# Performance work log

Hardware: AMD Instinct MI355X
Metric: run time of the kernel (lower is better)

The kernel has to match this reference:

```python
import jax, jax.numpy as jnp
import numpy as np

BLOCK_SIZE = 1024
DILATIONS = (1, 2, 4, 8)


def setup_inputs() -> dict:
    key = jax.random.key(0)
    kq, kk, kv, kw, kb = jax.random.split(key, 5)
    b, h, L, hd = 4, 8, 4096, 64
    hidden = h * hd
    return {
        "query_states": jax.random.normal(kq, (b, h, L, hd), jnp.float32),
        "key_states": jax.random.normal(kk, (b, h, L, hd), jnp.float32),
        "value_states": jax.random.normal(kv, (b, h, L, hd), jnp.float32),
        "Wo": jax.random.normal(kw, (hidden, hidden), jnp.float32),
        "bo": jax.random.normal(kb, (hidden,), jnp.float32),
    }


def _dilated_branch(q, k, v, d):
    """One dilation pass: strided gather -> block attention.
    Returns de (bsz, nh, Ld, 1) detached exp-row-sums and a (bsz, nh, Ld, hd)."""
    b, h, L, hd = q.shape
    qs, ks, vs = q[:, :, ::d], k[:, :, ::d], v[:, :, ::d]
    Ld = qs.shape[2]
    bs = min(BLOCK_SIZE, Ld)          # torch.split: one short block if Ld < block_size
    nb = Ld // bs                      # even split for chosen q_len
    blk = lambda x: x.reshape(b, h, nb, bs, hd)
    qb, kb, vb = blk(qs), blk(ks), blk(vs)
    scores = jnp.einsum('bhnqd,bhnkd->bhnqk', qb, kb) / jnp.sqrt(jnp.float32(hd))
    # detached, unstabilized exp-sum (matches attn_weights.detach().exp().sum(-1))
    de = jax.lax.stop_gradient(jnp.exp(scores).sum(-1, keepdims=True)).reshape(b, h, Ld, 1)
    probs = jax.nn.softmax(scores.astype(jnp.float32), axis=-1).astype(q.dtype)
    a = jnp.einsum('bhnqk,bhnkd->bhnqd', probs, vb).reshape(b, h, Ld, hd)
    return de, a


def reference(query_states, key_states, value_states, Wo, bo):
    b, h, L, hd = query_states.shape
    w = jnp.zeros((b, h, L, 1), jnp.float32)
    des, rs = [], []
    for d in DILATIONS:
        de, a = _dilated_branch(query_states, key_states, value_states, d)
        des.append(de)
        rs.append(a)
        w = w.at[:, :, ::d].add(de)
    out = jnp.zeros_like(query_states)
    for d, de, a in zip(DILATIONS, des, rs):
        aw = de / w[:, :, ::d]                     # (b, h, Ld, 1) relative weight
        out = out.at[:, :, ::d].add((aw * a).astype(query_states.dtype))
    out = out.transpose(0, 2, 1, 3).reshape(b, L, h * hd)
    return out @ Wo.T + bo
```

## Files before the change

kernel.cpp:

```cpp
#include <hip/hip_runtime.h>
#include <hip/hip_bf16.h>

typedef __attribute__((ext_vector_type(8))) short bf16x8;
typedef __attribute__((ext_vector_type(4))) float f32x4;
typedef unsigned short u16;

union F8 { bf16x8 v; unsigned u[4]; u16 s[8]; uint4 q; };

__device__ __forceinline__ unsigned pk2(float a, float b) {
    __hip_bfloat162 t = __float22bfloat162_rn(make_float2(a, b));
    unsigned r; __builtin_memcpy(&r, &t, 4); return r;
}
__device__ __forceinline__ u16 f2bf(float a) {
    __hip_bfloat16 t = __float2bfloat16(a);
    u16 r; __builtin_memcpy(&r, &t, 2); return r;
}
__device__ __forceinline__ float bf2f(u16 s) {
    unsigned u = ((unsigned)s) << 16; float f; __builtin_memcpy(&f, &u, 4); return f;
}
#define SWZ(byteoff, row) ((byteoff) ^ (((row) & 7) << 4))
#define MFMA(a, b, c) __builtin_amdgcn_mfma_f32_16x16x32_bf16((a), (b), (c), 0, 0, 0)

__global__ __launch_bounds__(256)
void prep_kernel(const float* __restrict__ K, const float* __restrict__ V,
                 u16* __restrict__ Kb, u16* __restrict__ Vt)
{
    __shared__ __align__(16) char tl[64 * 128];
    int blk = blockIdx.x;
    const int t = threadIdx.x;

    if (blk < 2048) {
        const int bh = blk >> 6, qt = blk & 63;
        const int q = qt * 64 + (t >> 2), dd0 = (t & 3) * 16;
        const float* kp = K + ((size_t)bh * 4096 + q) * 64 + dd0;
        float4 x0 = ((const float4*)kp)[0], x1 = ((const float4*)kp)[1];
        float4 x2 = ((const float4*)kp)[2], x3 = ((const float4*)kp)[3];
        F8 f0, f1;
        f0.u[0] = pk2(x0.x, x0.y); f0.u[1] = pk2(x0.z, x0.w);
        f0.u[2] = pk2(x1.x, x1.y); f0.u[3] = pk2(x1.z, x1.w);
        f1.u[0] = pk2(x2.x, x2.y); f1.u[1] = pk2(x2.z, x2.w);
        f1.u[2] = pk2(x3.x, x3.y); f1.u[3] = pk2(x3.z, x3.w);
        u16* op = Kb + ((size_t)bh * 4096 + q) * 64 + dd0;
        ((uint4*)op)[0] = f0.q; ((uint4*)op)[1] = f1.q;
        return;
    }
    blk -= 2048;
    int d, Ld; size_t vtoff;
    if (blk < 2048)      { d = 1; Ld = 4096; vtoff = 0; }
    else if (blk < 3072) { blk -= 2048; d = 2; Ld = 2048; vtoff = 8388608; }
    else if (blk < 3584) { blk -= 3072; d = 4; Ld = 1024; vtoff = 12582912; }
    else                 { blk -= 3584; d = 8; Ld = 512;  vtoff = 14680064; }
    const int tpb = Ld >> 6;
    const int bh = blk / tpb, jt = blk % tpb;
    {
        const int j = t >> 2, dd0 = (t & 3) * 16;
        const int q = (jt * 64 + j) * d;
        const float* vp = V + ((size_t)bh * 4096 + q) * 64 + dd0;
        float4 x0 = ((const float4*)vp)[0], x1 = ((const float4*)vp)[1];
        float4 x2 = ((const float4*)vp)[2], x3 = ((const float4*)vp)[3];
        F8 f0, f1;
        f0.u[0] = pk2(x0.x, x0.y); f0.u[1] = pk2(x0.z, x0.w);
        f0.u[2] = pk2(x1.x, x1.y); f0.u[3] = pk2(x1.z, x1.w);
        f1.u[0] = pk2(x2.x, x2.y); f1.u[1] = pk2(x2.z, x2.w);
        f1.u[2] = pk2(x3.x, x3.y); f1.u[3] = pk2(x3.z, x3.w);
        *(uint4*)(tl + SWZ(j * 128 + dd0 * 2, j)) = f0.q;
        *(uint4*)(tl + SWZ(j * 128 + dd0 * 2 + 16, j)) = f1.q;
    }
    __syncthreads();
    {
        const int dd = t >> 2, jb = (t & 3) * 16;
        F8 f0, f1;
#pragma unroll
        for (int i = 0; i < 8; ++i) {
            f0.s[i] = *(const u16*)(tl + SWZ((jb + i) * 128 + dd * 2, jb + i));
            f1.s[i] = *(const u16*)(tl + SWZ((jb + 8 + i) * 128 + dd * 2, jb + 8 + i));
        }
        u16* op = Vt + vtoff + ((size_t)bh * 64 + dd) * Ld + jt * 64 + jb;
        ((uint4*)op)[0] = f0.q; ((uint4*)op)[1] = f1.q;
    }
}

__global__ __launch_bounds__(256)
void attn_fused(const float* __restrict__ Q, const u16* __restrict__ Kb,
                const u16* __restrict__ Vt, float* __restrict__ num,
                float* __restrict__ wsum)
{
    const int L = 4096;
    const int per = gridDim.x >> 3;
    const int wg0 = blockIdx.x;
    const int wg = (wg0 & 7) * per + (wg0 >> 3);

    int d, npb, bs, rel; size_t vtoff;
    if (wg < 1024)      { d = 1; npb = 32; bs = 1024; rel = wg;        vtoff = 0; }
    else if (wg < 1536) { d = 2; npb = 16; bs = 1024; rel = wg - 1024; vtoff = 8388608; }
    else if (wg < 1792) { d = 4; npb = 8;  bs = 1024; rel = wg - 1536; vtoff = 12582912; }
    else                { d = 8; npb = 4;  bs = 512;  rel = wg - 1792; vtoff = 14680064; }

    const int bh = rel / npb;
    const int qt = rel % npb;
    const int b = bh >> 3, h = bh & 7;
    const int tid = threadIdx.x;
    const int w = tid >> 6, lane = tid & 63;
    const int g = lane >> 4, c = lane & 15;
    const int bstart = ((qt * 128) / bs) * bs;
    const int qrow0 = qt * 128 + w * 32;
    const int Ld = npb * 128;

    __shared__ __align__(16) char smem[32 * 1024];
    char* const Kls = smem;
    char* const Vls = smem + 8192;
    char* const Pls = smem + 16384 + w * 4096;

    const size_t base = (size_t)bh * L * 64;
    const size_t vbase = vtoff + (size_t)bh * 64 * Ld;
    const float qs = 0.125f * 1.44269504088896341f;

    bf16x8 qf[2][2];
#pragma unroll
    for (int qi = 0; qi < 2; ++qi) {
        const float* qp = Q + base + (size_t)(qrow0 + qi * 16 + c) * d * 64 + g * 8;
#pragma unroll
        for (int s = 0; s < 2; ++s) {
            float4 x = ((const float4*)(qp + s * 32))[0];
            float4 y = ((const float4*)(qp + s * 32))[1];
            F8 f;
            f.u[0] = pk2(x.x * qs, x.y * qs);
            f.u[1] = pk2(x.z * qs, x.w * qs);
            f.u[2] = pk2(y.x * qs, y.y * qs);
            f.u[3] = pk2(y.z * qs, y.w * qs);
            qf[qi][s] = f.v;
        }
    }

    f32x4 o[2][4];
#pragma unroll
    for (int qi = 0; qi < 2; ++qi)
#pragma unroll
        for (int dj = 0; dj < 4; ++dj) o[qi][dj] = (f32x4){0.f, 0.f, 0.f, 0.f};
    float lrow[2] = {0.f, 0.f};

    const int krow = tid >> 2, kc = tid & 3;

    uint4 ka, kb2, va, vb;
    {
        const u16* kp = Kb + base + (size_t)(bstart + krow) * d * 64 + kc * 16;
        ka = ((const uint4*)kp)[0]; kb2 = ((const uint4*)kp)[1];
        const u16* vp = Vt + vbase + (size_t)lane * Ld + bstart + w * 16;
        va = ((const uint4*)vp)[0]; vb = ((const uint4*)vp)[1];
    }

    for (int kt = 0; kt < bs; kt += 64) {
        *(uint4*)(Kls + SWZ(krow * 128 + kc * 32, krow)) = ka;
        *(uint4*)(Kls + SWZ(krow * 128 + kc * 32 + 16, krow)) = kb2;
        *(uint4*)(Vls + SWZ(lane * 128 + w * 32, lane)) = va;
        *(uint4*)(Vls + SWZ(lane * 128 + w * 32 + 16, lane)) = vb;
        __syncthreads();

        if (kt + 64 < bs) {
            const u16* kp = Kb + base + (size_t)(bstart + kt + 64 + krow) * d * 64 + kc * 16;
            ka = ((const uint4*)kp)[0]; kb2 = ((const uint4*)kp)[1];
            const u16* vp = Vt + vbase + (size_t)lane * Ld + bstart + kt + 64 + w * 16;
            va = ((const uint4*)vp)[0]; vb = ((const uint4*)vp)[1];
        }

        f32x4 st[2][4];
#pragma unroll
        for (int kj = 0; kj < 4; ++kj) {
            const int row = 16 * kj + c;
            bf16x8 kf0 = *(const bf16x8*)(Kls + SWZ(row * 128 + g * 16, row));
            bf16x8 kf1 = *(const bf16x8*)(Kls + SWZ(row * 128 + 64 + g * 16, row));
            f32x4 z = (f32x4){0.f, 0.f, 0.f, 0.f};
            st[0][kj] = MFMA(kf1, qf[0][1], MFMA(kf0, qf[0][0], z));
            st[1][kj] = MFMA(kf1, qf[1][1], MFMA(kf0, qf[1][0], z));
        }

#pragma unroll
        for (int qi = 0; qi < 2; ++qi) {
            const int prow = 16 * qi + c;
            float rs = 0.f;
#pragma unroll
            for (int kj = 0; kj < 4; ++kj) {
                const float p0 = exp2f(st[qi][kj][0]);
                const float p1 = exp2f(st[qi][kj][1]);
                const float p2 = exp2f(st[qi][kj][2]);
                const float p3 = exp2f(st[qi][kj][3]);
                rs += (p0 + p1) + (p2 + p3);
                uint2 pv; pv.x = pk2(p0, p1); pv.y = pk2(p2, p3);
                *(uint2*)(Pls + SWZ(prow * 128 + kj * 32 + g * 8, prow)) = pv;
            }
            lrow[qi] += rs;
        }

#pragma unroll
        for (int s = 0; s < 2; ++s) {
            bf16x8 vf[4], pf[2];
#pragma unroll
            for (int dj = 0; dj < 4; ++dj) {
                const int row = 16 * dj + c;
                vf[dj] = *(const bf16x8*)(Vls + SWZ(row * 128 + s * 64 + g * 16, row));
            }
#pragma unroll
            for (int qi = 0; qi < 2; ++qi) {
                const int row = 16 * qi + c;
                pf[qi] = *(const bf16x8*)(Pls + SWZ(row * 128 + s * 64 + g * 16, row));
            }
#pragma unroll
            for (int qi = 0; qi < 2; ++qi)
#pragma unroll
                for (int dj = 0; dj < 4; ++dj)
                    o[qi][dj] = MFMA(pf[qi], vf[dj], o[qi][dj]);
        }
        __syncthreads();
    }

#pragma unroll
    for (int qi = 0; qi < 2; ++qi) {
        float lq = lrow[qi];
        lq += __shfl_xor(lq, 16);
        lq += __shfl_xor(lq, 32);
#pragma unroll
        for (int r = 0; r < 4; ++r) {
            const int q = qrow0 + 16 * qi + 4 * g + r;
            float* np = num + ((size_t)b * L + (size_t)q * d) * 512 + h * 64 + c;
#pragma unroll
            for (int dj = 0; dj < 4; ++dj)
                atomicAdd(np + dj * 16, o[qi][dj][r]);
        }
        if (g == 0) {
            const int q2 = qrow0 + 16 * qi + c;
            atomicAdd(wsum + ((size_t)b * L + (size_t)q2 * d) * 8 + h, lq);
        }
    }
}

__global__ __launch_bounds__(256)
void proj_mfma(const float* __restrict__ num, const float* __restrict__ wsum,
               const float* __restrict__ Wo, const float* __restrict__ bo,
               float* __restrict__ out)
{
    __shared__ __align__(16) char smem[64 * 1024];
    char* const Ah = smem;
    char* const Al = smem + 16384;
    char* const Bh = smem + 32768;
    char* const Bl = smem + 49152;

    const int tid = threadIdx.x;
    const int w = tid >> 6, lane = tid & 63, g = lane >> 4, c = lane & 15;
    const int wm = (w >> 1) * 64, wn = (w & 1) * 64;
    const int per = gridDim.x >> 3;
    const int wg0 = blockIdx.x;
    const int wg = (wg0 & 7) * per + (wg0 >> 3);
    const int bm = (wg >> 2) * 128, bn = (wg & 3) * 128;
    const int srow = tid >> 1, koff = (tid & 1) * 32;

    f32x4 acc[4][4];
#pragma unroll
    for (int mi = 0; mi < 4; ++mi)
#pragma unroll
        for (int ni = 0; ni < 4; ++ni) acc[mi][ni] = (f32x4){0.f, 0.f, 0.f, 0.f};

    for (int bk = 0; bk < 512; bk += 64) {
        {
            const float* ap = num + (size_t)(bm + srow) * 512 + bk + koff;
            const float winv = 1.0f / wsum[(size_t)(bm + srow) * 8 + (bk >> 6)];
#pragma unroll
            for (int i = 0; i < 8; ++i) {
                float4 a4 = ((const float4*)ap)[i];
                float v0 = a4.x * winv, v1 = a4.y * winv, v2 = a4.z * winv, v3 = a4.w * winv;
                u16 h0 = f2bf(v0), h1 = f2bf(v1), h2 = f2bf(v2), h3 = f2bf(v3);
                uint2 hi; hi.x = h0 | ((unsigned)h1 << 16); hi.y = h2 | ((unsigned)h3 << 16);
                uint2 lo;
                lo.x = f2bf(v0 - bf2f(h0)) | ((unsigned)f2bf(v1 - bf2f(h1)) << 16);
                lo.y = f2bf(v2 - bf2f(h2)) | ((unsigned)f2bf(v3 - bf2f(h3)) << 16);
                const int off = SWZ(srow * 128 + koff * 2 + i * 8, srow);
                *(uint2*)(Ah + off) = hi;
                *(uint2*)(Al + off) = lo;
            }
            const float* bp = Wo + (size_t)(bn + srow) * 512 + bk + koff;
#pragma unroll
            for (int i = 0; i < 8; ++i) {
                float4 a4 = ((const float4*)bp)[i];
                u16 h0 = f2bf(a4.x), h1 = f2bf(a4.y), h2 = f2bf(a4.z), h3 = f2bf(a4.w);
                uint2 hi; hi.x = h0 | ((unsigned)h1 << 16); hi.y = h2 | ((unsigned)h3 << 16);
                uint2 lo;
                lo.x = f2bf(a4.x - bf2f(h0)) | ((unsigned)f2bf(a4.y - bf2f(h1)) << 16);
                lo.y = f2bf(a4.z - bf2f(h2)) | ((unsigned)f2bf(a4.w - bf2f(h3)) << 16);
                const int off = SWZ(srow * 128 + koff * 2 + i * 8, srow);
                *(uint2*)(Bh + off) = hi;
                *(uint2*)(Bl + off) = lo;
            }
        }
        __syncthreads();
#pragma unroll
        for (int s = 0; s < 2; ++s) {
            bf16x8 ah[4], al[4], bh[4], bl[4];
#pragma unroll
            for (int mi = 0; mi < 4; ++mi) {
                const int row = wm + 16 * mi + c;
                const int off = SWZ(row * 128 + s * 64 + g * 16, row);
                ah[mi] = *(const bf16x8*)(Ah + off);
                al[mi] = *(const bf16x8*)(Al + off);
            }
#pragma unroll
            for (int ni = 0; ni < 4; ++ni) {
                const int row = wn + 16 * ni + c;
                const int off = SWZ(row * 128 + s * 64 + g * 16, row);
                bh[ni] = *(const bf16x8*)(Bh + off);
                bl[ni] = *(const bf16x8*)(Bl + off);
            }
#pragma unroll
            for (int mi = 0; mi < 4; ++mi)
#pragma unroll
                for (int ni = 0; ni < 4; ++ni) {
                    acc[mi][ni] = MFMA(ah[mi], bh[ni], acc[mi][ni]);
                    acc[mi][ni] = MFMA(ah[mi], bl[ni], acc[mi][ni]);
                    acc[mi][ni] = MFMA(al[mi], bh[ni], acc[mi][ni]);
                }
        }
        __syncthreads();
    }

    float bias[4];
#pragma unroll
    for (int ni = 0; ni < 4; ++ni) bias[ni] = bo[bn + wn + 16 * ni + c];
#pragma unroll
    for (int mi = 0; mi < 4; ++mi)
#pragma unroll
        for (int r = 0; r < 4; ++r) {
            float* op = out + (size_t)(bm + wm + 16 * mi + 4 * g + r) * 512 + bn + wn + c;
#pragma unroll
            for (int ni = 0; ni < 4; ++ni)
                op[ni * 16] = acc[mi][ni][r] + bias[ni];
        }
}

extern "C" void kernel_launch(void* const* d_in, const int* in_sizes, int n_in,
                              void* d_out, int out_size, void* d_ws, size_t ws_size,
                              hipStream_t stream)
{
    const float* Q  = (const float*)d_in[0];
    const float* K  = (const float*)d_in[1];
    const float* V  = (const float*)d_in[2];
    const float* Wo = (const float*)d_in[3];
    const float* bo = (const float*)d_in[4];
    float* out = (float*)d_out;

    float* num  = (float*)d_ws;
    float* wsum = num + (size_t)8388608;
    u16*  Kb    = (u16*)((char*)d_ws + 34078720);
    u16*  Vt    = (u16*)((char*)d_ws + 50855936);

    hipMemsetAsync(d_ws, 0, 34078720, stream);

    hipLaunchKernelGGL(prep_kernel, dim3(5888), dim3(256), 0, stream, K, V, Kb, Vt);
    hipLaunchKernelGGL(attn_fused, dim3(1920), dim3(256), 0, stream,
                       Q, Kb, Vt, num, wsum);
    hipLaunchKernelGGL(proj_mfma, dim3(512), dim3(256), 0, stream,
                       num, wsum, Wo, bo, out);
}
```

Before: 217.5 us.

## Switch attention to 32x32x16 MFMA with register P shuffle and double-buffered LDS

Rewrites the attention inner loop to use 32x32x16 bf16 MFMA tiles. The probability tile is now passed from the QK^T result into the PV operand through lane shuffles instead of a round trip through LDS. K/V LDS tiles are double-buffered with prefetch two steps ahead, leaving a single barrier per iteration. The aim is fewer LDS writes and reads, fewer MFMA issues, and fewer barriers. The cost is larger accumulator register use, extra shuffle/select work, and a different atomic write-out pattern.

```diff
diff --git a/kernel.cpp b/kernel.cpp
--- a/kernel.cpp
+++ b/kernel.cpp
@@ -3,6 +3,7 @@
 
 typedef __attribute__((ext_vector_type(8))) short bf16x8;
 typedef __attribute__((ext_vector_type(4))) float f32x4;
+typedef __attribute__((ext_vector_type(16))) float f32x16;
 typedef unsigned short u16;
 
 union F8 { bf16x8 v; unsigned u[4]; u16 s[8]; uint4 q; };
@@ -20,6 +21,7 @@
 }
 #define SWZ(byteoff, row) ((byteoff) ^ (((row) & 7) << 4))
 #define MFMA(a, b, c) __builtin_amdgcn_mfma_f32_16x16x32_bf16((a), (b), (c), 0, 0, 0)
+#define MFMA32(a, b, c) __builtin_amdgcn_mfma_f32_32x32x16_bf16((a), (b), (c), 0, 0, 0)
 
 __global__ __launch_bounds__(256)
 void prep_kernel(const float* __restrict__ K, const float* __restrict__ V,
@@ -101,136 +103,152 @@
     const int b = bh >> 3, h = bh & 7;
     const int tid = threadIdx.x;
     const int w = tid >> 6, lane = tid & 63;
-    const int g = lane >> 4, c = lane & 15;
+    const int lq = lane & 31;
+    const int hi = lane >> 5;
     const int bstart = ((qt * 128) / bs) * bs;
     const int qrow0 = qt * 128 + w * 32;
     const int Ld = npb * 128;
+    const int nt = bs >> 6;
 
     __shared__ __align__(16) char smem[32 * 1024];
-    char* const Kls = smem;
-    char* const Vls = smem + 8192;
-    char* const Pls = smem + 16384 + w * 4096;
-
     const size_t base = (size_t)bh * L * 64;
     const size_t vbase = vtoff + (size_t)bh * 64 * Ld;
     const float qs = 0.125f * 1.44269504088896341f;
 
-    bf16x8 qf[2][2];
-#pragma unroll
-    for (int qi = 0; qi < 2; ++qi) {
-        const float* qp = Q + base + (size_t)(qrow0 + qi * 16 + c) * d * 64 + g * 8;
-#pragma unroll
-        for (int s = 0; s < 2; ++s) {
-            float4 x = ((const float4*)(qp + s * 32))[0];
-            float4 y = ((const float4*)(qp + s * 32))[1];
+    bf16x8 qb[4];
+    {
+        const float* qp = Q + base + (size_t)(qrow0 + lq) * d * 64 + hi * 8;
+#pragma unroll
+        for (int ks = 0; ks < 4; ++ks) {
+            float4 x = ((const float4*)(qp + ks * 16))[0];
+            float4 y = ((const float4*)(qp + ks * 16))[1];
             F8 f;
             f.u[0] = pk2(x.x * qs, x.y * qs);
             f.u[1] = pk2(x.z * qs, x.w * qs);
             f.u[2] = pk2(y.x * qs, y.y * qs);
             f.u[3] = pk2(y.z * qs, y.w * qs);
-            qf[qi][s] = f.v;
-        }
-    }
-
-    f32x4 o[2][4];
-#pragma unroll
-    for (int qi = 0; qi < 2; ++qi)
-#pragma unroll
-        for (int dj = 0; dj < 4; ++dj) o[qi][dj] = (f32x4){0.f, 0.f, 0.f, 0.f};
-    float lrow[2] = {0.f, 0.f};
+            qb[ks] = f.v;
+        }
+    }
+
+    f32x16 o0, o1;
+#pragma unroll
+    for (int i = 0; i < 16; ++i) { o0[i] = 0.f; o1[i] = 0.f; }
+    float lrow = 0.f;
 
     const int krow = tid >> 2, kc = tid & 3;
 
     uint4 ka, kb2, va, vb;
+    const u16* kp0 = Kb + base + (size_t)(bstart + krow) * d * 64 + kc * 16;
+    const u16* vp0 = Vt + vbase + (size_t)lane * Ld + bstart + w * 16;
+    const size_t kstep = (size_t)64 * d * 64;
+
+    ka = ((const uint4*)kp0)[0]; kb2 = ((const uint4*)kp0)[1];
+    va = ((const uint4*)vp0)[0]; vb = ((const uint4*)vp0)[1];
     {
-        const u16* kp = Kb + base + (size_t)(bstart + krow) * d * 64 + kc * 16;
-        ka = ((const uint4*)kp)[0]; kb2 = ((const uint4*)kp)[1];
-        const u16* vp = Vt + vbase + (size_t)lane * Ld + bstart + w * 16;
-        va = ((const uint4*)vp)[0]; vb = ((const uint4*)vp)[1];
-    }
-
-    for (int kt = 0; kt < bs; kt += 64) {
+        char* Kls = smem; char* Vls = smem + 8192;
         *(uint4*)(Kls + SWZ(krow * 128 + kc * 32, krow)) = ka;
         *(uint4*)(Kls + SWZ(krow * 128 + kc * 32 + 16, krow)) = kb2;
         *(uint4*)(Vls + SWZ(lane * 128 + w * 32, lane)) = va;
         *(uint4*)(Vls + SWZ(lane * 128 + w * 32 + 16, lane)) = vb;
+    }
+    if (nt > 1) {
+        ka = ((const uint4*)(kp0 + kstep))[0]; kb2 = ((const uint4*)(kp0 + kstep))[1];
+        va = ((const uint4*)(vp0 + 64))[0];    vb = ((const uint4*)(vp0 + 64))[1];
+    }
+    __syncthreads();
+
+    for (int t = 0; t < nt; ++t) {
+        char* const Kls = smem + (t & 1) * 16384;
+        char* const Vls = Kls + 8192;
+        if (t + 1 < nt) {
+            char* Klsn = smem + ((t + 1) & 1) * 16384;
+            char* Vlsn = Klsn + 8192;
+            *(uint4*)(Klsn + SWZ(krow * 128 + kc * 32, krow)) = ka;
+            *(uint4*)(Klsn + SWZ(krow * 128 + kc * 32 + 16, krow)) = kb2;
+            *(uint4*)(Vlsn + SWZ(lane * 128 + w * 32, lane)) = va;
+            *(uint4*)(Vlsn + SWZ(lane * 128 + w * 32 + 16, lane)) = vb;
+        }
+        if (t + 2 < nt) {
+            const u16* kp = kp0 + (size_t)(t + 2) * kstep;
+            const u16* vp = vp0 + (t + 2) * 64;
+            ka = ((const uint4*)kp)[0]; kb2 = ((const uint4*)kp)[1];
+            va = ((const uint4*)vp)[0]; vb = ((const uint4*)vp)[1];
+        }
+
+        f32x16 st0, st1;
+#pragma unroll
+        for (int i = 0; i < 16; ++i) { st0[i] = 0.f; st1[i] = 0.f; }
+#pragma unroll
+        for (int ks = 0; ks < 4; ++ks) {
+            bf16x8 kf0 = *(const bf16x8*)(Kls + SWZ(lq * 128 + ks * 32 + hi * 16, lq));
+            bf16x8 kf1 = *(const bf16x8*)(Kls + SWZ((32 + lq) * 128 + ks * 32 + hi * 16, 32 + lq));
+            st0 = MFMA32(kf0, qb[ks], st0);
+            st1 = MFMA32(kf1, qb[ks], st1);
+        }
+
+        f32x16 p0, p1;
+        float rs = 0.f;
+#pragma unroll
+        for (int r = 0; r < 16; ++r) {
+            p0[r] = exp2f(st0[r]); p1[r] = exp2f(st1[r]);
+            rs += p0[r] + p1[r];
+        }
+        lrow += rs;
+
+        bf16x8 pa[4];
+        {
+            unsigned u0 = pk2(p0[0], p0[1]),   u1 = pk2(p0[2], p0[3]);
+            unsigned u2 = pk2(p0[4], p0[5]),   u3 = pk2(p0[6], p0[7]);
+            unsigned u4 = pk2(p0[8], p0[9]),   u5 = pk2(p0[10], p0[11]);
+            unsigned u6 = pk2(p0[12], p0[13]), u7 = pk2(p0[14], p0[15]);
+            unsigned t0 = __shfl_xor(u0, 32), t1 = __shfl_xor(u1, 32);
+            unsigned t2 = __shfl_xor(u2, 32), t3 = __shfl_xor(u3, 32);
+            unsigned t4 = __shfl_xor(u4, 32), t5 = __shfl_xor(u5, 32);
+            unsigned t6 = __shfl_xor(u6, 32), t7 = __shfl_xor(u7, 32);
+            F8 f;
+            f.u[0] = hi ? t2 : u0; f.u[1] = hi ? t3 : u1;
+            f.u[2] = hi ? u2 : t0; f.u[3] = hi ? u3 : t1;
+            pa[0] = f.v;
+            f.u[0] = hi ? t6 : u4; f.u[1] = hi ? t7 : u5;
+            f.u[2] = hi ? u6 : t4; f.u[3] = hi ? u7 : t5;
+            pa[1] = f.v;
+            u0 = pk2(p1[0], p1[1]);   u1 = pk2(p1[2], p1[3]);
+            u2 = pk2(p1[4], p1[5]);   u3 = pk2(p1[6], p1[7]);
+            u4 = pk2(p1[8], p1[9]);   u5 = pk2(p1[10], p1[11]);
+            u6 = pk2(p1[12], p1[13]); u7 = pk2(p1[14], p1[15]);
+            t0 = __shfl_xor(u0, 32); t1 = __shfl_xor(u1, 32);
+            t2 = __shfl_xor(u2, 32); t3 = __shfl_xor(u3, 32);
+            t4 = __shfl_xor(u4, 32); t5 = __shfl_xor(u5, 32);
+            t6 = __shfl_xor(u6, 32); t7 = __shfl_xor(u7, 32);
+            f.u[0] = hi ? t2 : u0; f.u[1] = hi ? t3 : u1;
+            f.u[2] = hi ? u2 : t0; f.u[3] = hi ? u3 : t1;
+            pa[2] = f.v;
+            f.u[0] = hi ? t6 : u4; f.u[1] = hi ? t7 : u5;
+            f.u[2] = hi ? u6 : t4; f.u[3] = hi ? u7 : t5;
+            pa[3] = f.v;
+        }
+
+#pragma unroll
+        for (int ks = 0; ks < 4; ++ks) {
+            bf16x8 v0 = *(const bf16x8*)(Vls + SWZ(lq * 128 + ks * 32 + hi * 16, lq));
+            bf16x8 v1 = *(const bf16x8*)(Vls + SWZ((32 + lq) * 128 + ks * 32 + hi * 16, 32 + lq));
+            o0 = MFMA32(pa[ks], v0, o0);
+            o1 = MFMA32(pa[ks], v1, o1);
+        }
         __syncthreads();
-
-        if (kt + 64 < bs) {
-            const u16* kp = Kb + base + (size_t)(bstart + kt + 64 + krow) * d * 64 + kc * 16;
-            ka = ((const uint4*)kp)[0]; kb2 = ((const uint4*)kp)[1];
-            const u16* vp = Vt + vbase + (size_t)lane * Ld + bstart + kt + 64 + w * 16;
-            va = ((const uint4*)vp)[0]; vb = ((const uint4*)vp)[1];
-        }
-
-        f32x4 st[2][4];
-#pragma unroll
-        for (int kj = 0; kj < 4; ++kj) {
-            const int row = 16 * kj + c;
-            bf16x8 kf0 = *(const bf16x8*)(Kls + SWZ(row * 128 + g * 16, row));
-            bf16x8 kf1 = *(const bf16x8*)(Kls + SWZ(row * 128 + 64 + g * 16, row));
-            f32x4 z = (f32x4){0.f, 0.f, 0.f, 0.f};
-            st[0][kj] = MFMA(kf1, qf[0][1], MFMA(kf0, qf[0][0], z));
-            st[1][kj] = MFMA(kf1, qf[1][1], MFMA(kf0, qf[1][0], z));
-        }
-
-#pragma unroll
-        for (int qi = 0; qi < 2; ++qi) {
-            const int prow = 16 * qi + c;
-            float rs = 0.f;
-#pragma unroll
-            for (int kj = 0; kj < 4; ++kj) {
-                const float p0 = exp2f(st[qi][kj][0]);
-                const float p1 = exp2f(st[qi][kj][1]);
-                const float p2 = exp2f(st[qi][kj][2]);
-                const float p3 = exp2f(st[qi][kj][3]);
-                rs += (p0 + p1) + (p2 + p3);
-                uint2 pv; pv.x = pk2(p0, p1); pv.y = pk2(p2, p3);
-                *(uint2*)(Pls + SWZ(prow * 128 + kj * 32 + g * 8, prow)) = pv;
-            }
-            lrow[qi] += rs;
-        }
-
-#pragma unroll
-        for (int s = 0; s < 2; ++s) {
-            bf16x8 vf[4], pf[2];
-#pragma unroll
-            for (int dj = 0; dj < 4; ++dj) {
-                const int row = 16 * dj + c;
-                vf[dj] = *(const bf16x8*)(Vls + SWZ(row * 128 + s * 64 + g * 16, row));
-            }
-#pragma unroll
-            for (int qi = 0; qi < 2; ++qi) {
-                const int row = 16 * qi + c;
-                pf[qi] = *(const bf16x8*)(Pls + SWZ(row * 128 + s * 64 + g * 16, row));
-            }
-#pragma unroll
-            for (int qi = 0; qi < 2; ++qi)
-#pragma unroll
-                for (int dj = 0; dj < 4; ++dj)
-                    o[qi][dj] = MFMA(pf[qi], vf[dj], o[qi][dj]);
-        }
-        __syncthreads();
-    }
-
-#pragma unroll
-    for (int qi = 0; qi < 2; ++qi) {
-        float lq = lrow[qi];
-        lq += __shfl_xor(lq, 16);
-        lq += __shfl_xor(lq, 32);
-#pragma unroll
-        for (int r = 0; r < 4; ++r) {
-            const int q = qrow0 + 16 * qi + 4 * g + r;
-            float* np = num + ((size_t)b * L + (size_t)q * d) * 512 + h * 64 + c;
-#pragma unroll
-            for (int dj = 0; dj < 4; ++dj)
-                atomicAdd(np + dj * 16, o[qi][dj][r]);
-        }
-        if (g == 0) {
-            const int q2 = qrow0 + 16 * qi + c;
-            atomicAdd(wsum + ((size_t)b * L + (size_t)q2 * d) * 8 + h, lq);
-        }
-    }
+    }
+
+    float lsum = lrow + __shfl_xor(lrow, 32);
+#pragma unroll
+    for (int r = 0; r < 16; ++r) {
+        const int qr = (r & 3) + 8 * (r >> 2) + 4 * hi;
+        float* np = num + ((size_t)b * L + (size_t)(qrow0 + qr) * d) * 512 + h * 64 + lq;
+        atomicAdd(np, o0[r]);
+        atomicAdd(np + 32, o1[r]);
+    }
+    if (lane < 32)
+        atomicAdd(wsum + ((size_t)b * L + (size_t)(qrow0 + lq) * d) * 8 + h, lsum);
 }
 
 __global__ __launch_bounds__(256)
@@ -268,12 +286,12 @@
                 float4 a4 = ((const float4*)ap)[i];
                 float v0 = a4.x * winv, v1 = a4.y * winv, v2 = a4.z * winv, v3 = a4.w * winv;
                 u16 h0 = f2bf(v0), h1 = f2bf(v1), h2 = f2bf(v2), h3 = f2bf(v3);
-                uint2 hi; hi.x = h0 | ((unsigned)h1 << 16); hi.y = h2 | ((unsigned)h3 << 16);
+                uint2 hiw; hiw.x = h0 | ((unsigned)h1 << 16); hiw.y = h2 | ((unsigned)h3 << 16);
                 uint2 lo;
                 lo.x = f2bf(v0 - bf2f(h0)) | ((unsigned)f2bf(v1 - bf2f(h1)) << 16);
                 lo.y = f2bf(v2 - bf2f(h2)) | ((unsigned)f2bf(v3 - bf2f(h3)) << 16);
                 const int off = SWZ(srow * 128 + koff * 2 + i * 8, srow);
-                *(uint2*)(Ah + off) = hi;
+                *(uint2*)(Ah + off) = hiw;
                 *(uint2*)(Al + off) = lo;
             }
             const float* bp = Wo + (size_t)(bn + srow) * 512 + bk + koff;
@@ -281,12 +299,12 @@
             for (int i = 0; i < 8; ++i) {
                 float4 a4 = ((const float4*)bp)[i];
                 u16 h0 = f2bf(a4.x), h1 = f2bf(a4.y), h2 = f2bf(a4.z), h3 = f2bf(a4.w);
-                uint2 hi; hi.x = h0 | ((unsigned)h1 << 16); hi.y = h2 | ((unsigned)h3 << 16);
+                uint2 hiw; hiw.x = h0 | ((unsigned)h1 << 16); hiw.y = h2 | ((unsigned)h3 << 16);
                 uint2 lo;
                 lo.x = f2bf(a4.x - bf2f(h0)) | ((unsigned)f2bf(a4.y - bf2f(h1)) << 16);
                 lo.y = f2bf(a4.z - bf2f(h2)) | ((unsigned)f2bf(a4.w - bf2f(h3)) << 16);
                 const int off = SWZ(srow * 128 + koff * 2 + i * 8, srow);
-                *(uint2*)(Bh + off) = hi;
+                *(uint2*)(Bh + off) = hiw;
                 *(uint2*)(Bl + off) = lo;
             }
         }
```

Result: slower. 243.0 us (+11.7%).

## Double per-workgroup query tile to 256 rows to halve K/V reloads

Applied to the files above, without the earlier changes.

Each workgroup now handles 256 query rows (64 per wave) instead of 128, so the grid halves to 960 and each K/V tile staged in shared memory is reused by twice as many queries. The S=QK^T and exp step is split into two 32-key halves to limit register pressure, and the P buffer per wave grows to 8 KB, taking LDS to 48 KB. This cuts global/L2 traffic and barrier count per query, but raises register and LDS use, which lowers occupancy, and leaves fewer workgroups to fill the GPU.

```diff
diff --git a/kernel.cpp b/kernel.cpp
--- a/kernel.cpp
+++ b/kernel.cpp
@@ -91,10 +91,10 @@
     const int wg = (wg0 & 7) * per + (wg0 >> 3);
 
     int d, npb, bs, rel; size_t vtoff;
-    if (wg < 1024)      { d = 1; npb = 32; bs = 1024; rel = wg;        vtoff = 0; }
-    else if (wg < 1536) { d = 2; npb = 16; bs = 1024; rel = wg - 1024; vtoff = 8388608; }
-    else if (wg < 1792) { d = 4; npb = 8;  bs = 1024; rel = wg - 1536; vtoff = 12582912; }
-    else                { d = 8; npb = 4;  bs = 512;  rel = wg - 1792; vtoff = 14680064; }
+    if (wg < 512)      { d = 1; npb = 16; bs = 1024; rel = wg;       vtoff = 0; }
+    else if (wg < 768) { d = 2; npb = 8;  bs = 1024; rel = wg - 512; vtoff = 8388608; }
+    else if (wg < 896) { d = 4; npb = 4;  bs = 1024; rel = wg - 768; vtoff = 12582912; }
+    else               { d = 8; npb = 2;  bs = 512;  rel = wg - 896; vtoff = 14680064; }
 
     const int bh = rel / npb;
     const int qt = rel % npb;
@@ -102,110 +102,114 @@
     const int tid = threadIdx.x;
     const int w = tid >> 6, lane = tid & 63;
     const int g = lane >> 4, c = lane & 15;
-    const int bstart = ((qt * 128) / bs) * bs;
-    const int qrow0 = qt * 128 + w * 32;
-    const int Ld = npb * 128;
-
-    __shared__ __align__(16) char smem[32 * 1024];
+    const int bstart = ((qt * 256) / bs) * bs;
+    const int qrow0 = qt * 256 + w * 64;
+    const int Ld = npb * 256;
+    const int nt = bs >> 6;
+
+    __shared__ __align__(16) char smem[48 * 1024];
     char* const Kls = smem;
     char* const Vls = smem + 8192;
-    char* const Pls = smem + 16384 + w * 4096;
+    char* const Pls = smem + 16384 + w * 8192;
 
     const size_t base = (size_t)bh * L * 64;
     const size_t vbase = vtoff + (size_t)bh * 64 * Ld;
     const float qs = 0.125f * 1.44269504088896341f;
 
-    bf16x8 qf[2][2];
-#pragma unroll
-    for (int qi = 0; qi < 2; ++qi) {
+    bf16x8 qf[4][2];
+#pragma unroll
+    for (int qi = 0; qi < 4; ++qi) {
         const float* qp = Q + base + (size_t)(qrow0 + qi * 16 + c) * d * 64 + g * 8;
 #pragma unroll
-        for (int s = 0; s < 2; ++s) {
-            float4 x = ((const float4*)(qp + s * 32))[0];
-            float4 y = ((const float4*)(qp + s * 32))[1];
+        for (int s2 = 0; s2 < 2; ++s2) {
+            float4 x = ((const float4*)(qp + s2 * 32))[0];
+            float4 y = ((const float4*)(qp + s2 * 32))[1];
             F8 f;
             f.u[0] = pk2(x.x * qs, x.y * qs);
             f.u[1] = pk2(x.z * qs, x.w * qs);
             f.u[2] = pk2(y.x * qs, y.y * qs);
             f.u[3] = pk2(y.z * qs, y.w * qs);
-            qf[qi][s] = f.v;
-        }
-    }
-
-    f32x4 o[2][4];
-#pragma unroll
-    for (int qi = 0; qi < 2; ++qi)
+            qf[qi][s2] = f.v;
+        }
+    }
+
+    f32x4 o[4][4];
+#pragma unroll
+    for (int qi = 0; qi < 4; ++qi)
 #pragma unroll
         for (int dj = 0; dj < 4; ++dj) o[qi][dj] = (f32x4){0.f, 0.f, 0.f, 0.f};
-    float lrow[2] = {0.f, 0.f};
+    float lrow[4] = {0.f, 0.f, 0.f, 0.f};
 
     const int krow = tid >> 2, kc = tid & 3;
 
     uint4 ka, kb2, va, vb;
-    {
-        const u16* kp = Kb + base + (size_t)(bstart + krow) * d * 64 + kc * 16;
-        ka = ((const uint4*)kp)[0]; kb2 = ((const uint4*)kp)[1];
-        const u16* vp = Vt + vbase + (size_t)lane * Ld + bstart + w * 16;
-        va = ((const uint4*)vp)[0]; vb = ((const uint4*)vp)[1];
-    }
-
-    for (int kt = 0; kt < bs; kt += 64) {
+    const u16* kp0 = Kb + base + (size_t)(bstart + krow) * d * 64 + kc * 16;
+    const u16* vp0 = Vt + vbase + (size_t)lane * Ld + bstart + w * 16;
+    const size_t kstep = (size_t)64 * d * 64;
+    ka = ((const uint4*)kp0)[0]; kb2 = ((const uint4*)kp0)[1];
+    va = ((const uint4*)vp0)[0]; vb = ((const uint4*)vp0)[1];
+
+    for (int t = 0; t < nt; ++t) {
         *(uint4*)(Kls + SWZ(krow * 128 + kc * 32, krow)) = ka;
         *(uint4*)(Kls + SWZ(krow * 128 + kc * 32 + 16, krow)) = kb2;
         *(uint4*)(Vls + SWZ(lane * 128 + w * 32, lane)) = va;
         *(uint4*)(Vls + SWZ(lane * 128 + w * 32 + 16, lane)) = vb;
         __syncthreads();
 
-        if (kt + 64 < bs) {
-            const u16* kp = Kb + base + (size_t)(bstart + kt + 64 + krow) * d * 64 + kc * 16;
+        if (t + 1 < nt) {
+            const u16* kp = kp0 + (size_t)(t + 1) * kstep;
+            const u16* vp = vp0 + (t + 1) * 64;
             ka = ((const uint4*)kp)[0]; kb2 = ((const uint4*)kp)[1];
-            const u16* vp = Vt + vbase + (size_t)lane * Ld + bstart + kt + 64 + w * 16;
             va = ((const uint4*)vp)[0]; vb = ((const uint4*)vp)[1];
         }
 
-        f32x4 st[2][4];
-#pragma unroll
-        for (int kj = 0; kj < 4; ++kj) {
-            const int row = 16 * kj + c;
-            bf16x8 kf0 = *(const bf16x8*)(Kls + SWZ(row * 128 + g * 16, row));
-            bf16x8 kf1 = *(const bf16x8*)(Kls + SWZ(row * 128 + 64 + g * 16, row));
-            f32x4 z = (f32x4){0.f, 0.f, 0.f, 0.f};
-            st[0][kj] = MFMA(kf1, qf[0][1], MFMA(kf0, qf[0][0], z));
-            st[1][kj] = MFMA(kf1, qf[1][1], MFMA(kf0, qf[1][0], z));
-        }
-
-#pragma unroll
-        for (int qi = 0; qi < 2; ++qi) {
-            const int prow = 16 * qi + c;
-            float rs = 0.f;
-#pragma unroll
-            for (int kj = 0; kj < 4; ++kj) {
-                const float p0 = exp2f(st[qi][kj][0]);
-                const float p1 = exp2f(st[qi][kj][1]);
-                const float p2 = exp2f(st[qi][kj][2]);
-                const float p3 = exp2f(st[qi][kj][3]);
-                rs += (p0 + p1) + (p2 + p3);
-                uint2 pv; pv.x = pk2(p0, p1); pv.y = pk2(p2, p3);
-                *(uint2*)(Pls + SWZ(prow * 128 + kj * 32 + g * 8, prow)) = pv;
-            }
-            lrow[qi] += rs;
-        }
-
 #pragma unroll
         for (int s = 0; s < 2; ++s) {
-            bf16x8 vf[4], pf[2];
+            f32x4 st[4][2];
+#pragma unroll
+            for (int kj = 0; kj < 2; ++kj) {
+                const int row = 32 * s + 16 * kj + c;
+                bf16x8 kf0 = *(const bf16x8*)(Kls + SWZ(row * 128 + g * 16, row));
+                bf16x8 kf1 = *(const bf16x8*)(Kls + SWZ(row * 128 + 64 + g * 16, row));
+#pragma unroll
+                for (int qi = 0; qi < 4; ++qi) {
+                    f32x4 z = (f32x4){0.f, 0.f, 0.f, 0.f};
+                    st[qi][kj] = MFMA(kf1, qf[qi][1], MFMA(kf0, qf[qi][0], z));
+                }
+            }
+#pragma unroll
+            for (int qi = 0; qi < 4; ++qi) {
+                const int prow = 16 * qi + c;
+                float rs = 0.f;
+#pragma unroll
+                for (int kj = 0; kj < 2; ++kj) {
+                    const float p0 = exp2f(st[qi][kj][0]);
+                    const float p1 = exp2f(st[qi][kj][1]);
+                    const float p2 = exp2f(st[qi][kj][2]);
+                    const float p3 = exp2f(st[qi][kj][3]);
+                    rs += (p0 + p1) + (p2 + p3);
+                    uint2 pv; pv.x = pk2(p0, p1); pv.y = pk2(p2, p3);
+                    *(uint2*)(Pls + SWZ(prow * 128 + s * 64 + kj * 32 + g * 8, prow)) = pv;
+                }
+                lrow[qi] += rs;
+            }
+        }
+
+#pragma unroll
+        for (int s = 0; s < 2; ++s) {
+            bf16x8 vf[4], pf[4];
 #pragma unroll
             for (int dj = 0; dj < 4; ++dj) {
                 const int row = 16 * dj + c;
                 vf[dj] = *(const bf16x8*)(Vls + SWZ(row * 128 + s * 64 + g * 16, row));
             }
 #pragma unroll
-            for (int qi = 0; qi < 2; ++qi) {
+            for (int qi = 0; qi < 4; ++qi) {
                 const int row = 16 * qi + c;
                 pf[qi] = *(const bf16x8*)(Pls + SWZ(row * 128 + s * 64 + g * 16, row));
             }
 #pragma unroll
-            for (int qi = 0; qi < 2; ++qi)
+            for (int qi = 0; qi < 4; ++qi)
 #pragma unroll
                 for (int dj = 0; dj < 4; ++dj)
                     o[qi][dj] = MFMA(pf[qi], vf[dj], o[qi][dj]);
@@ -214,7 +218,7 @@
     }
 
 #pragma unroll
-    for (int qi = 0; qi < 2; ++qi) {
+    for (int qi = 0; qi < 4; ++qi) {
         float lq = lrow[qi];
         lq += __shfl_xor(lq, 16);
         lq += __shfl_xor(lq, 32);
@@ -268,12 +272,12 @@
                 float4 a4 = ((const float4*)ap)[i];
                 float v0 = a4.x * winv, v1 = a4.y * winv, v2 = a4.z * winv, v3 = a4.w * winv;
                 u16 h0 = f2bf(v0), h1 = f2bf(v1), h2 = f2bf(v2), h3 = f2bf(v3);
-                uint2 hi; hi.x = h0 | ((unsigned)h1 << 16); hi.y = h2 | ((unsigned)h3 << 16);
+                uint2 hiw; hiw.x = h0 | ((unsigned)h1 << 16); hiw.y = h2 | ((unsigned)h3 << 16);
                 uint2 lo;
                 lo.x = f2bf(v0 - bf2f(h0)) | ((unsigned)f2bf(v1 - bf2f(h1)) << 16);
                 lo.y = f2bf(v2 - bf2f(h2)) | ((unsigned)f2bf(v3 - bf2f(h3)) << 16);
                 const int off = SWZ(srow * 128 + koff * 2 + i * 8, srow);
-                *(uint2*)(Ah + off) = hi;
+                *(uint2*)(Ah + off) = hiw;
                 *(uint2*)(Al + off) = lo;
             }
             const float* bp = Wo + (size_t)(bn + srow) * 512 + bk + koff;
@@ -281,12 +285,12 @@
             for (int i = 0; i < 8; ++i) {
                 float4 a4 = ((const float4*)bp)[i];
                 u16 h0 = f2bf(a4.x), h1 = f2bf(a4.y), h2 = f2bf(a4.z), h3 = f2bf(a4.w);
-                uint2 hi; hi.x = h0 | ((unsigned)h1 << 16); hi.y = h2 | ((unsigned)h3 << 16);
+                uint2 hiw; hiw.x = h0 | ((unsigned)h1 << 16); hiw.y = h2 | ((unsigned)h3 << 16);
                 uint2 lo;
                 lo.x = f2bf(a4.x - bf2f(h0)) | ((unsigned)f2bf(a4.y - bf2f(h1)) << 16);
                 lo.y = f2bf(a4.z - bf2f(h2)) | ((unsigned)f2bf(a4.w - bf2f(h3)) << 16);
                 const int off = SWZ(srow * 128 + koff * 2 + i * 8, srow);
-                *(uint2*)(Bh + off) = hi;
+                *(uint2*)(Bh + off) = hiw;
                 *(uint2*)(Bl + off) = lo;
             }
         }
@@ -353,7 +357,7 @@
     hipMemsetAsync(d_ws, 0, 34078720, stream);
 
     hipLaunchKernelGGL(prep_kernel, dim3(5888), dim3(256), 0, stream, K, V, Kb, Vt);
-    hipLaunchKernelGGL(attn_fused, dim3(1920), dim3(256), 0, stream,
+    hipLaunchKernelGGL(attn_fused, dim3(960), dim3(256), 0, stream,
                        Q, Kb, Vt, num, wsum);
     hipLaunchKernelGGL(proj_mfma, dim3(512), dim3(256), 0, stream,
                        num, wsum, Wo, bo, out);
```

Measured after the change: 295.1 us. +35.7%, slower.
